# Performance work log

Measured on AMD Instinct MI355X. Metric: run time of the kernel, lower is better.

Reference implementation:

```python
import jax, jax.numpy as jnp
import numpy as np


def setup_inputs() -> dict:
    key = jax.random.key(0)
    ks = jax.random.split(key, 5)
    B, H, W, C, R = 4, 64, 64, 256, 32
    x = jax.random.normal(ks[0], (B, H, W, C), dtype=jnp.float32)
    # 1x1 conv kernels stored as [C_in, C_out] matrices (equivalent math)
    w_f = jax.random.normal(ks[1], (C, R), dtype=jnp.float32) * (1.0 / np.sqrt(C))
    w_g = jax.random.normal(ks[2], (C, R), dtype=jnp.float32) * (1.0 / np.sqrt(C))
    w_h = jax.random.normal(ks[3], (C, R), dtype=jnp.float32) * (1.0 / np.sqrt(C))
    w_v = jax.random.normal(ks[4], (R, C), dtype=jnp.float32) * (1.0 / np.sqrt(R))
    gamma = jnp.zeros((1,), dtype=jnp.float32)
    return {"x": x, "w_f": w_f, "w_g": w_g, "w_h": w_h, "w_v": w_v, "gamma": gamma}


def reference(x, w_f, w_g, w_h, w_v, gamma):
    B, H, W, C = x.shape
    N = H * W
    xt = x.reshape(B, N, C)                       # flatten spatial tokens
    f = jnp.einsum('bnc,cr->bnr', xt, w_f)        # 1x1 conv == token-wise matmul
    g = jnp.einsum('bnc,cr->bnr', xt, w_g)
    h = jnp.einsum('bnc,cr->bnr', xt, w_h)
    scores = jnp.einsum('bnr,bmr->bnm', f, g)     # [B, N, N]
    # NOTE: original softmaxes over axis=1 (the query/row axis), not axis=-1
    attn = jax.nn.softmax(scores, axis=1)
    y = jnp.einsum('bnm,bmr->bnr', attn, h)       # [B, N, R]
    y = jnp.einsum('bnr,rc->bnc', y, w_v)         # output 1x1 conv
    y = y.reshape(B, H, W, C)
    return gamma * y + x
```

## Files before the change

kernel.cpp:

```cpp
#include <hip/hip_runtime.h>


#define BB 4
#define NN 4096
#define CC 256
#define RR 32
#define CSEG 4
#define PSEG 4
#define PPAD 40

typedef short short8 __attribute__((ext_vector_type(8)));
typedef float floatx4 __attribute__((ext_vector_type(4)));

#define MFMA16 __builtin_amdgcn_mfma_f32_16x16x32_bf16

static __device__ __forceinline__ unsigned short f2bf(float f) {
  union { float f; unsigned u; } v; v.f = f;
  const unsigned r = v.u + 0x7fffu + ((v.u >> 16) & 1u);
  return (unsigned short)(r >> 16);
}

__global__ __launch_bounds__(256) void k_prep(
    const float* __restrict__ wf, const float* __restrict__ wg,
    const float* __restrict__ wh, const float* __restrict__ wv,
    unsigned short* __restrict__ wfrag, unsigned short* __restrict__ wvfrag) {
  const int idx = blockIdx.x * 256 + threadIdx.x;
  const int lane = (idx >> 3) & 63;
  const int j = idx & 7;
  const int col = lane & 15, q = lane >> 4;
  if (idx < 24576) {
    const int mat = idx >> 13;
    const int fid = (idx >> 9) & 15;
    const int kc = fid >> 1, nt = fid & 1;
    const float* w = (mat == 0) ? wf : ((mat == 1) ? wg : wh);
    wfrag[idx] = f2bf(w[(kc * 32 + q * 8 + j) * RR + nt * 16 + col]);
  } else {
    const int r = idx - 24576;
    const int t = (r >> 9) & 15;
    wvfrag[r] = f2bf(wv[(q * 8 + j) * CC + t * 16 + col]);
  }
}

__global__ __launch_bounds__(256) void k_fgh(
    const float* __restrict__ x, const unsigned short* __restrict__ wfrag,
    unsigned short* __restrict__ f16, unsigned short* __restrict__ g16,
    unsigned short* __restrict__ hT16) {
  const int tid = threadIdx.x, lane = tid & 63, wave = tid >> 6;
  const int col = lane & 15, q = lane >> 4;
  const int t0 = blockIdx.x * 64 + wave * 16;
  short8 af[8];
  const float* xr = x + (long)(t0 + col) * CC + q * 8;
#pragma unroll
  for (int kc = 0; kc < 8; ++kc) {
    float tmp[8];
    *(float4*)(tmp) = *(const float4*)(xr + kc * 32);
    *(float4*)(tmp + 4) = *(const float4*)(xr + kc * 32 + 4);
    short8 o;
#pragma unroll
    for (int j = 0; j < 8; ++j) o[j] = (short)f2bf(tmp[j]);
    af[kc] = o;
  }
  const floatx4 zero = {0.f, 0.f, 0.f, 0.f};
  floatx4 acc[3][2];
#pragma unroll
  for (int m = 0; m < 3; ++m) { acc[m][0] = zero; acc[m][1] = zero; }
  const short8* wfr = (const short8*)wfrag;
#pragma unroll
  for (int kc = 0; kc < 8; ++kc) {
#pragma unroll
    for (int mat = 0; mat < 3; ++mat) {
#pragma unroll
      for (int nt = 0; nt < 2; ++nt) {
        const short8 bf = wfr[(mat * 16 + kc * 2 + nt) * 64 + lane];
        acc[mat][nt] = MFMA16(af[kc], bf, acc[mat][nt], 0, 0, 0);
      }
    }
  }
  const int b = t0 >> 12;
#pragma unroll
  for (int nt = 0; nt < 2; ++nt) {
#pragma unroll
    for (int r = 0; r < 4; ++r) {
      const int tok = t0 + q * 4 + r;
      const int n = nt * 16 + col;
      f16[(long)tok * RR + n] = f2bf(acc[0][nt][r]);
      g16[(long)tok * RR + n] = f2bf(acc[1][nt][r]);
      hT16[((long)b * RR + n) * NN + (tok & (NN - 1))] = f2bf(acc[2][nt][r]);
    }
  }
}

__global__ __launch_bounds__(256) void k_colsum(
    const unsigned short* __restrict__ f16, const unsigned short* __restrict__ g16,
    float* __restrict__ psum) {
  const int tid = threadIdx.x, lane = tid & 63, wave = tid >> 6;
  const int col = lane & 15, q = lane >> 4;
  const int mblk = blockIdx.x & 31;
  const int b = (blockIdx.x >> 5) & 3;
  const int seg = blockIdx.x >> 7;
  const int m0 = mblk * 128 + wave * 32;
  const short8 bg1 = *(const short8*)(g16 + ((long)(b * NN + m0 + col)) * RR + q * 8);
  const short8 bg2 = *(const short8*)(g16 + ((long)(b * NN + m0 + 16 + col)) * RR + q * 8);
  const floatx4 zero = {0.f, 0.f, 0.f, 0.f};
  float s1 = 0.f, s2 = 0.f;
  const unsigned short* fb = f16 + ((long)b * NN + seg * (NN / CSEG)) * RR;
#pragma unroll 4
  for (int n = 0; n < NN / CSEG; n += 16) {
    const short8 af = *(const short8*)(fb + (long)(n + col) * RR + q * 8);
    const floatx4 d1 = MFMA16(af, bg1, zero, 0, 0, 0);
    const floatx4 d2 = MFMA16(af, bg2, zero, 0, 0, 0);
    s1 += __expf(d1[0]) + __expf(d1[1]) + __expf(d1[2]) + __expf(d1[3]);
    s2 += __expf(d2[0]) + __expf(d2[1]) + __expf(d2[2]) + __expf(d2[3]);
  }
  s1 += __shfl_xor(s1, 16); s1 += __shfl_xor(s1, 32);
  s2 += __shfl_xor(s2, 16); s2 += __shfl_xor(s2, 32);
  if (lane < 16) {
    psum[(long)seg * (BB * NN) + b * NN + m0 + lane] = s1;
    psum[(long)seg * (BB * NN) + b * NN + m0 + 16 + lane] = s2;
  }
}

__global__ __launch_bounds__(256) void k_redsum(
    const float* __restrict__ psum, float* __restrict__ ci) {
  const int m = blockIdx.x * 256 + threadIdx.x;
  float s = 0.f;
#pragma unroll
  for (int sg = 0; sg < CSEG; ++sg) s += psum[(long)sg * (BB * NN) + m];
  ci[m] = 1.0f / s;
}

__global__ __launch_bounds__(256) void k_pv(
    const unsigned short* __restrict__ f16, const unsigned short* __restrict__ g16,
    const unsigned short* __restrict__ hT16, const float* __restrict__ ci,
    float* __restrict__ py) {
  __shared__ unsigned short pt_all[4][32 * PPAD];
  __shared__ float cis[NN / PSEG];
  const int tid = threadIdx.x, lane = tid & 63, wave = tid >> 6;
  const int col = lane & 15, q = lane >> 4;
  const int nblk = blockIdx.x & 31;
  const int b = (blockIdx.x >> 5) & 3;
  const int mseg = blockIdx.x >> 7;
  const int n0 = nblk * 128 + wave * 32;
  const int mbase = mseg * (NN / PSEG);
  for (int i = tid; i < NN / PSEG; i += 256) cis[i] = ci[b * NN + mbase + i];
  __syncthreads();
  const short8 af1 = *(const short8*)(f16 + ((long)(b * NN + n0 + col)) * RR + q * 8);
  const short8 af2 = *(const short8*)(f16 + ((long)(b * NN + n0 + 16 + col)) * RR + q * 8);
  const floatx4 zero = {0.f, 0.f, 0.f, 0.f};
  floatx4 a11 = zero, a12 = zero, a21 = zero, a22 = zero;
  unsigned short* pt = &pt_all[wave][0];
  const unsigned short* gb = g16 + (long)b * NN * RR;
  const unsigned short* hb = hT16 + (long)b * RR * NN;
  for (int mi = 0; mi < NN / PSEG; mi += 32) {
    const int m0 = mbase + mi;
    const short8 bg1 = *(const short8*)(gb + (long)(m0 + col) * RR + q * 8);
    const short8 bg2 = *(const short8*)(gb + (long)(m0 + 16 + col) * RR + q * 8);
    const floatx4 d11 = MFMA16(af1, bg1, zero, 0, 0, 0);
    const floatx4 d12 = MFMA16(af1, bg2, zero, 0, 0, 0);
    const floatx4 d21 = MFMA16(af2, bg1, zero, 0, 0, 0);
    const floatx4 d22 = MFMA16(af2, bg2, zero, 0, 0, 0);
    const float c1 = cis[mi + col];
    const float c2 = cis[mi + 16 + col];
#pragma unroll
    for (int r = 0; r < 4; ++r) {
      pt[(q * 4 + r) * PPAD + col]           = f2bf(__expf(d11[r]) * c1);
      pt[(q * 4 + r) * PPAD + col + 16]      = f2bf(__expf(d12[r]) * c2);
      pt[(q * 4 + r + 16) * PPAD + col]      = f2bf(__expf(d21[r]) * c1);
      pt[(q * 4 + r + 16) * PPAD + col + 16] = f2bf(__expf(d22[r]) * c2);
    }
    const short8 ap1 = *(const short8*)(pt + col * PPAD + q * 8);
    const short8 ap2 = *(const short8*)(pt + (col + 16) * PPAD + q * 8);
    const short8 bh1 = *(const short8*)(hb + (long)col * NN + m0 + q * 8);
    const short8 bh2 = *(const short8*)(hb + (long)(col + 16) * NN + m0 + q * 8);
    a11 = MFMA16(ap1, bh1, a11, 0, 0, 0);
    a12 = MFMA16(ap1, bh2, a12, 0, 0, 0);
    a21 = MFMA16(ap2, bh1, a21, 0, 0, 0);
    a22 = MFMA16(ap2, bh2, a22, 0, 0, 0);
  }
  float* yp = py + (long)(mseg * BB + b) * NN * RR;
#pragma unroll
  for (int r = 0; r < 4; ++r) {
    yp[(long)(n0 + q * 4 + r) * RR + col]           = a11[r];
    yp[(long)(n0 + q * 4 + r) * RR + col + 16]      = a12[r];
    yp[(long)(n0 + 16 + q * 4 + r) * RR + col]      = a21[r];
    yp[(long)(n0 + 16 + q * 4 + r) * RR + col + 16] = a22[r];
  }
}

__global__ __launch_bounds__(256) void k_out(
    const float* __restrict__ py, const unsigned short* __restrict__ wvfrag,
    const float* __restrict__ x, const float* __restrict__ gamma,
    float* __restrict__ out) {
  const int tid = threadIdx.x, lane = tid & 63, wave = tid >> 6;
  const int col = lane & 15, q = lane >> 4;
  const int t0 = blockIdx.x * 64 + wave * 16;
  const int b = t0 >> 12;
  const int tloc = t0 & (NN - 1);
  float s[8] = {0.f, 0.f, 0.f, 0.f, 0.f, 0.f, 0.f, 0.f};
#pragma unroll
  for (int sg = 0; sg < PSEG; ++sg) {
    const float* p = py + ((long)(sg * BB + b) * NN + tloc + col) * RR + q * 8;
    const float4 u0 = *(const float4*)p;
    const float4 u1 = *(const float4*)(p + 4);
    s[0] += u0.x; s[1] += u0.y; s[2] += u0.z; s[3] += u0.w;
    s[4] += u1.x; s[5] += u1.y; s[6] += u1.z; s[7] += u1.w;
  }
  short8 ay;
#pragma unroll
  for (int j = 0; j < 8; ++j) ay[j] = (short)f2bf(s[j]);
  const float gm = gamma[0];
  const floatx4 zero = {0.f, 0.f, 0.f, 0.f};
  const short8* wvf = (const short8*)wvfrag;
#pragma unroll
  for (int t = 0; t < 16; ++t) {
    const short8 bw = wvf[t * 64 + lane];
    const floatx4 d = MFMA16(ay, bw, zero, 0, 0, 0);
#pragma unroll
    for (int r = 0; r < 4; ++r) {
      const long idx = (long)(t0 + q * 4 + r) * CC + t * 16 + col;
      out[idx] = gm * d[r] + x[idx];
    }
  }
}

extern "C" void kernel_launch(void* const* d_in, const int* in_sizes, int n_in,
                              void* d_out, int out_size, void* d_ws, size_t ws_size,
                              hipStream_t stream) {
  const float* x = (const float*)d_in[0];
  const float* wf = (const float*)d_in[1];
  const float* wg = (const float*)d_in[2];
  const float* wh = (const float*)d_in[3];
  const float* wv = (const float*)d_in[4];
  const float* gamma = (const float*)d_in[5];
  float* out = (float*)d_out;

  unsigned short* wfrag = (unsigned short*)d_ws;
  unsigned short* wvfrag = wfrag + 24576;
  unsigned short* f16 = wvfrag + 8192;
  unsigned short* g16 = f16 + (long)BB * NN * RR;
  unsigned short* hT16 = g16 + (long)BB * NN * RR;
  float* psum = (float*)(hT16 + (long)BB * NN * RR);
  float* ci = psum + (long)CSEG * BB * NN;
  float* py = ci + (long)BB * NN;

  k_prep<<<128, 256, 0, stream>>>(wf, wg, wh, wv, wfrag, wvfrag);
  k_fgh<<<BB * NN / 64, 256, 0, stream>>>(x, wfrag, f16, g16, hT16);
  k_colsum<<<CSEG * BB * 32, 256, 0, stream>>>(f16, g16, psum);
  k_redsum<<<BB * NN / 256, 256, 0, stream>>>(psum, ci);
  k_pv<<<PSEG * BB * 32, 256, 0, stream>>>(f16, g16, hT16, ci, py);
  k_out<<<BB * NN / 64, 256, 0, stream>>>(py, wvfrag, x, gamma, out);
}
```

Measured before the change: 147.4 us.

## Fold log2e into f, fuse redsum into pv, vectorize P and output stores

Pre-scales f by log2(e) so the exponentials become raw exp2 instructions. The separate reciprocal-sum kernel is removed and each k_pv block reduces the partial column sums itself. The P-tile MFMA operands are swapped so each lane writes four packed bf16 values in one 8-byte LDS store. k_out stages results through LDS so the x loads and output stores become coalesced float4 accesses. The costs are redundant psum reduction across n-blocks and extra LDS traffic in k_out.

```diff
diff --git a/kernel.cpp b/kernel.cpp
--- a/kernel.cpp
+++ b/kernel.cpp
@@ -7,7 +7,8 @@
 #define RR 32
 #define CSEG 4
 #define PSEG 4
-#define PPAD 40
+#define MP 40
+#define LOG2E 1.44269504088896340736f
 
 typedef short short8 __attribute__((ext_vector_type(8)));
 typedef float floatx4 __attribute__((ext_vector_type(4)));
@@ -18,6 +19,9 @@
   union { float f; unsigned u; } v; v.f = f;
   const unsigned r = v.u + 0x7fffu + ((v.u >> 16) & 1u);
   return (unsigned short)(r >> 16);
+}
+static __device__ __forceinline__ unsigned bfpack(float lo, float hi) {
+  return __builtin_amdgcn_perm(__float_as_uint(hi), __float_as_uint(lo), 0x07060302u);
 }
 
 __global__ __launch_bounds__(256) void k_prep(
@@ -83,7 +87,7 @@
     for (int r = 0; r < 4; ++r) {
       const int tok = t0 + q * 4 + r;
       const int n = nt * 16 + col;
-      f16[(long)tok * RR + n] = f2bf(acc[0][nt][r]);
+      f16[(long)tok * RR + n] = f2bf(acc[0][nt][r] * LOG2E);
       g16[(long)tok * RR + n] = f2bf(acc[1][nt][r]);
       hT16[((long)b * RR + n) * NN + (tok & (NN - 1))] = f2bf(acc[2][nt][r]);
     }
@@ -109,8 +113,10 @@
     const short8 af = *(const short8*)(fb + (long)(n + col) * RR + q * 8);
     const floatx4 d1 = MFMA16(af, bg1, zero, 0, 0, 0);
     const floatx4 d2 = MFMA16(af, bg2, zero, 0, 0, 0);
-    s1 += __expf(d1[0]) + __expf(d1[1]) + __expf(d1[2]) + __expf(d1[3]);
-    s2 += __expf(d2[0]) + __expf(d2[1]) + __expf(d2[2]) + __expf(d2[3]);
+    s1 += __builtin_amdgcn_exp2f(d1[0]) + __builtin_amdgcn_exp2f(d1[1]) +
+          __builtin_amdgcn_exp2f(d1[2]) + __builtin_amdgcn_exp2f(d1[3]);
+    s2 += __builtin_amdgcn_exp2f(d2[0]) + __builtin_amdgcn_exp2f(d2[1]) +
+          __builtin_amdgcn_exp2f(d2[2]) + __builtin_amdgcn_exp2f(d2[3]);
   }
   s1 += __shfl_xor(s1, 16); s1 += __shfl_xor(s1, 32);
   s2 += __shfl_xor(s2, 16); s2 += __shfl_xor(s2, 32);
@@ -120,20 +126,12 @@
   }
 }
 
-__global__ __launch_bounds__(256) void k_redsum(
-    const float* __restrict__ psum, float* __restrict__ ci) {
-  const int m = blockIdx.x * 256 + threadIdx.x;
-  float s = 0.f;
-#pragma unroll
-  for (int sg = 0; sg < CSEG; ++sg) s += psum[(long)sg * (BB * NN) + m];
-  ci[m] = 1.0f / s;
-}
-
+#define C_ADDR(TN, TM) (((TN) + col) * MP + (TM) + q * 4)
 __global__ __launch_bounds__(256) void k_pv(
     const unsigned short* __restrict__ f16, const unsigned short* __restrict__ g16,
-    const unsigned short* __restrict__ hT16, const float* __restrict__ ci,
+    const unsigned short* __restrict__ hT16, const float* __restrict__ psum,
     float* __restrict__ py) {
-  __shared__ unsigned short pt_all[4][32 * PPAD];
+  __shared__ unsigned short pt_all[4][32 * MP];
   __shared__ float cis[NN / PSEG];
   const int tid = threadIdx.x, lane = tid & 63, wave = tid >> 6;
   const int col = lane & 15, q = lane >> 4;
@@ -142,7 +140,12 @@
   const int mseg = blockIdx.x >> 7;
   const int n0 = nblk * 128 + wave * 32;
   const int mbase = mseg * (NN / PSEG);
-  for (int i = tid; i < NN / PSEG; i += 256) cis[i] = ci[b * NN + mbase + i];
+  for (int i = tid; i < NN / PSEG; i += 256) {
+    float s = 0.f;
+#pragma unroll
+    for (int sg = 0; sg < CSEG; ++sg) s += psum[(long)sg * (BB * NN) + b * NN + mbase + i];
+    cis[i] = 1.0f / s;
+  }
   __syncthreads();
   const short8 af1 = *(const short8*)(f16 + ((long)(b * NN + n0 + col)) * RR + q * 8);
   const short8 af2 = *(const short8*)(f16 + ((long)(b * NN + n0 + 16 + col)) * RR + q * 8);
@@ -155,21 +158,29 @@
     const int m0 = mbase + mi;
     const short8 bg1 = *(const short8*)(gb + (long)(m0 + col) * RR + q * 8);
     const short8 bg2 = *(const short8*)(gb + (long)(m0 + 16 + col) * RR + q * 8);
-    const floatx4 d11 = MFMA16(af1, bg1, zero, 0, 0, 0);
-    const floatx4 d12 = MFMA16(af1, bg2, zero, 0, 0, 0);
-    const floatx4 d21 = MFMA16(af2, bg1, zero, 0, 0, 0);
-    const floatx4 d22 = MFMA16(af2, bg2, zero, 0, 0, 0);
-    const float c1 = cis[mi + col];
-    const float c2 = cis[mi + 16 + col];
-#pragma unroll
-    for (int r = 0; r < 4; ++r) {
-      pt[(q * 4 + r) * PPAD + col]           = f2bf(__expf(d11[r]) * c1);
-      pt[(q * 4 + r) * PPAD + col + 16]      = f2bf(__expf(d12[r]) * c2);
-      pt[(q * 4 + r + 16) * PPAD + col]      = f2bf(__expf(d21[r]) * c1);
-      pt[(q * 4 + r + 16) * PPAD + col + 16] = f2bf(__expf(d22[r]) * c2);
-    }
-    const short8 ap1 = *(const short8*)(pt + col * PPAD + q * 8);
-    const short8 ap2 = *(const short8*)(pt + (col + 16) * PPAD + q * 8);
+    const floatx4 d00 = MFMA16(bg1, af1, zero, 0, 0, 0);
+    const floatx4 d01 = MFMA16(bg2, af1, zero, 0, 0, 0);
+    const floatx4 d10 = MFMA16(bg1, af2, zero, 0, 0, 0);
+    const floatx4 d11 = MFMA16(bg2, af2, zero, 0, 0, 0);
+    const float4 cia = *(const float4*)(cis + mi + q * 4);
+    const float4 cib = *(const float4*)(cis + mi + 16 + q * 4);
+    {
+      float w0, w1, w2, w3;
+      w0 = __builtin_amdgcn_exp2f(d00[0]) * cia.x; w1 = __builtin_amdgcn_exp2f(d00[1]) * cia.y;
+      w2 = __builtin_amdgcn_exp2f(d00[2]) * cia.z; w3 = __builtin_amdgcn_exp2f(d00[3]) * cia.w;
+      *(uint2*)(pt + C_ADDR(0, 0)) = make_uint2(bfpack(w0, w1), bfpack(w2, w3));
+      w0 = __builtin_amdgcn_exp2f(d01[0]) * cib.x; w1 = __builtin_amdgcn_exp2f(d01[1]) * cib.y;
+      w2 = __builtin_amdgcn_exp2f(d01[2]) * cib.z; w3 = __builtin_amdgcn_exp2f(d01[3]) * cib.w;
+      *(uint2*)(pt + C_ADDR(0, 16)) = make_uint2(bfpack(w0, w1), bfpack(w2, w3));
+      w0 = __builtin_amdgcn_exp2f(d10[0]) * cia.x; w1 = __builtin_amdgcn_exp2f(d10[1]) * cia.y;
+      w2 = __builtin_amdgcn_exp2f(d10[2]) * cia.z; w3 = __builtin_amdgcn_exp2f(d10[3]) * cia.w;
+      *(uint2*)(pt + C_ADDR(16, 0)) = make_uint2(bfpack(w0, w1), bfpack(w2, w3));
+      w0 = __builtin_amdgcn_exp2f(d11[0]) * cib.x; w1 = __builtin_amdgcn_exp2f(d11[1]) * cib.y;
+      w2 = __builtin_amdgcn_exp2f(d11[2]) * cib.z; w3 = __builtin_amdgcn_exp2f(d11[3]) * cib.w;
+      *(uint2*)(pt + C_ADDR(16, 16)) = make_uint2(bfpack(w0, w1), bfpack(w2, w3));
+    }
+    const short8 ap1 = *(const short8*)(pt + col * MP + q * 8);
+    const short8 ap2 = *(const short8*)(pt + (col + 16) * MP + q * 8);
     const short8 bh1 = *(const short8*)(hb + (long)col * NN + m0 + q * 8);
     const short8 bh2 = *(const short8*)(hb + (long)(col + 16) * NN + m0 + q * 8);
     a11 = MFMA16(ap1, bh1, a11, 0, 0, 0);
@@ -191,6 +202,7 @@
     const float* __restrict__ py, const unsigned short* __restrict__ wvfrag,
     const float* __restrict__ x, const float* __restrict__ gamma,
     float* __restrict__ out) {
+  __shared__ float ot[4][16 * 132];
   const int tid = threadIdx.x, lane = tid & 63, wave = tid >> 6;
   const int col = lane & 15, q = lane >> 4;
   const int t0 = blockIdx.x * 64 + wave * 16;
@@ -211,14 +223,26 @@
   const float gm = gamma[0];
   const floatx4 zero = {0.f, 0.f, 0.f, 0.f};
   const short8* wvf = (const short8*)wvfrag;
-#pragma unroll
-  for (int t = 0; t < 16; ++t) {
-    const short8 bw = wvf[t * 64 + lane];
-    const floatx4 d = MFMA16(ay, bw, zero, 0, 0, 0);
-#pragma unroll
-    for (int r = 0; r < 4; ++r) {
-      const long idx = (long)(t0 + q * 4 + r) * CC + t * 16 + col;
-      out[idx] = gm * d[r] + x[idx];
+  float* pw = &ot[wave][0];
+  const int tok = lane >> 2, cg = (lane & 3) * 4;
+#pragma unroll
+  for (int h = 0; h < 2; ++h) {
+#pragma unroll
+    for (int t = 0; t < 8; ++t) {
+      const short8 bw = wvf[(h * 8 + t) * 64 + lane];
+      const floatx4 d = MFMA16(ay, bw, zero, 0, 0, 0);
+#pragma unroll
+      for (int r = 0; r < 4; ++r) pw[(q * 4 + r) * 132 + t * 16 + col] = d[r];
+    }
+#pragma unroll
+    for (int j = 0; j < 8; ++j) {
+      const float4 v = *(const float4*)(pw + tok * 132 + cg + j * 16);
+      const long gidx = (long)(t0 + tok) * CC + h * 128 + cg + j * 16;
+      const float4 xv = *(const float4*)(x + gidx);
+      float4 o;
+      o.x = gm * v.x + xv.x; o.y = gm * v.y + xv.y;
+      o.z = gm * v.z + xv.z; o.w = gm * v.w + xv.w;
+      *(float4*)(out + gidx) = o;
     }
   }
 }
@@ -240,13 +264,11 @@
   unsigned short* g16 = f16 + (long)BB * NN * RR;
   unsigned short* hT16 = g16 + (long)BB * NN * RR;
   float* psum = (float*)(hT16 + (long)BB * NN * RR);
-  float* ci = psum + (long)CSEG * BB * NN;
-  float* py = ci + (long)BB * NN;
+  float* py = psum + (long)CSEG * BB * NN;
 
   k_prep<<<128, 256, 0, stream>>>(wf, wg, wh, wv, wfrag, wvfrag);
   k_fgh<<<BB * NN / 64, 256, 0, stream>>>(x, wfrag, f16, g16, hT16);
   k_colsum<<<CSEG * BB * 32, 256, 0, stream>>>(f16, g16, psum);
-  k_redsum<<<BB * NN / 256, 256, 0, stream>>>(psum, ci);
-  k_pv<<<PSEG * BB * 32, 256, 0, stream>>>(f16, g16, hT16, ci, py);
+  k_pv<<<PSEG * BB * 32, 256, 0, stream>>>(f16, g16, hT16, psum, py);
   k_out<<<BB * NN / 64, 256, 0, stream>>>(py, wvfrag, x, gamma, out);
 }
```

After: 131.7 us. 1.12x faster.
